# Kernel optimization log

Measured on AMD Instinct MI355X. Metric: run time of the kernel, lower is better.

Reference implementation:

```python
import jax, jax.numpy as jnp
import numpy as np

N_ATOMS = 100000
N_PAIRS = 4000000
N_TYPES = 200
# atom_description columns
AT_NAME, RESNUM, CHAIN = 0, 1, 2
# atom_Properties columns
P_CHARGED, P_CHARGE, P_VIRTUAL, P_DIPOLE, P_RADIUS = 0, 1, 2, 3, 4
# atom-name hash codes (stand-ins for hashings.atom_hash entries)
PHE_RC, TYR_RC, ARG_CZ, ARG_ARG = 10, 11, 12, 13
TEMPERATURE = 298.0
CONSTANT = float(np.exp(-0.004314 * (TEMPERATURE - 273.0)))
DIELEC = 8.8
ION_CORR = 0.02 + 0.05 / 1.4  # Ionic_corrected
PAD = 999.0  # PADDING_INDEX
MAX_DISTANCE = 15.0
KON_APPROACH = 6.0
SOLV_DIELEC = 88.0
RAD10 = float(np.radians(10.0))
RAD30 = float(np.radians(30.0))
RAD150 = float(np.radians(150.0))
RAD180 = float(np.radians(180.0))


def setup_inputs() -> dict:
    key = jax.random.key(0)
    k = jax.random.split(key, 10)
    coords = jax.random.normal(k[0], (N_ATOMS, 3), jnp.float32) * 10.0
    partners = jax.random.normal(k[1], (N_ATOMS, 2, 3), jnp.float32) * 10.0
    at_name = jax.random.randint(k[2], (N_ATOMS,), 0, N_TYPES)
    resnum = jax.random.randint(k[3], (N_ATOMS,), 0, 500)
    chain = jax.random.randint(k[4], (N_ATOMS,), 0, 4)
    atom_description = jnp.stack([at_name, resnum, chain], axis=-1)
    atomPairs = jax.random.randint(k[5], (N_PAIRS, 2), 0, N_ATOMS)
    charged = jax.random.bernoulli(k[6], 0.4, (N_TYPES,)).astype(jnp.float32)
    charge = jax.random.choice(k[7], jnp.array([-1.0, -0.5, 0.5, 1.0], jnp.float32), (N_TYPES,)) * charged
    virtual = jax.random.bernoulli(k[8], 0.1, (N_TYPES,)).astype(jnp.float32)
    kd, kr = jax.random.split(k[9])
    dipole = jax.random.bernoulli(kd, 0.3, (N_TYPES,)).astype(jnp.float32)
    radius = jax.random.uniform(kr, (N_TYPES,), jnp.float32, 1.2, 2.2)
    atom_Properties = jnp.stack([charged, charge, virtual, dipole, radius], axis=-1)
    return {"coords": coords, "partners": partners, "atom_Properties": atom_Properties,
            "atom_description": atom_description, "atomPairs": atomPairs}


def _electro_energy(coords, partners, atom_Properties, atom_description, atomPairs):
    i = atomPairs[:, 0]
    j = atomPairs[:, 1]
    at1 = atom_description[i, AT_NAME]
    at2 = atom_description[j, AT_NAME]

    rc1 = (at1 == PHE_RC) | (at1 == TYR_RC)
    rc2 = (at2 == PHE_RC) | (at2 == TYR_RC)
    argInvolved = ((at1 == ARG_CZ) & ((at2 == ARG_CZ) | rc2)) | ((at2 == ARG_CZ) & ((at1 == ARG_CZ) | rc1))

    charged1 = atom_Properties[at1, P_CHARGED] == 1
    charged2 = atom_Properties[at2, P_CHARGED] == 1
    # NcpMask/CcpMask are all-False (calculate_helical_dipoles == False branch)
    is_charged = (charged1 & charged2) | argInvolved

    diff = coords[i] - coords[j]
    dist = jnp.sqrt(jnp.sum(diff * diff, axis=-1) + 1e-12)  # [P]

    same_res = (atom_description[i, RESNUM] != atom_description[j, RESNUM]) | \
               (atom_description[i, CHAIN] != atom_description[j, CHAIN])
    valid = is_charged & (dist <= MAX_DISTANCE) & same_res  # is_charged_mask & first_mask

    c1 = atom_Properties[at1, P_CHARGE]
    c2 = atom_Properties[at2, P_CHARGE]
    v1 = atom_Properties[at1, P_VIRTUAL] == 1
    v2 = atom_Properties[at2, P_VIRTUAL] == 1
    # hDipoleInvolved is all-False, so the helix-dipole term contributes 0
    charged_charged = valid & (c1 != 0) & (c2 != 0) & (c1 != PAD) & (c2 != PAD) & (~v1) & (~v2)

    # ---- ARG stacking term (plane angle between the two guanidinium/ring planes)
    pA0 = partners[i, 0]; pA1 = partners[i, 1]; cA = coords[i]
    pB0 = partners[j, 0]; pB1 = partners[j, 1]; cB = coords[j]
    n1 = jnp.cross(pA0 - cA, pA1 - cA)
    n2 = jnp.cross(pB0 - cB, pB1 - cB)
    nn1 = jnp.sqrt(jnp.sum(n1 * n1, axis=-1) + 1e-12)
    nn2 = jnp.sqrt(jnp.sum(n2 * n2, axis=-1) + 1e-12)
    m = (nn1 > 1e-6) & (nn2 > 1e-6)
    cosang = jnp.clip(jnp.sum(n1 * n2, axis=-1) / (nn1 * nn2), -0.999999, 0.999999)
    ang = jnp.arccos(cosang)
    ang_bad = ((ang > RAD30) & (ang < RAD150)) | (dist < 3.9) | (dist > 4.3) | (~m)
    arg_mask = valid & argInvolved & (~ang_bad)

    dsafe = jnp.maximum(dist, 1e-6)
    argEpss = 332.0 / (dsafe * DIELEC * CONSTANT)
    temp_d = 3.0 + jnp.abs(dist - 4.1)
    angCorr = dist > RAD150  # faithful to source: distance compared against radians(150)
    corr_ang = jnp.where(angCorr,
                         jnp.maximum((RAD180 - ang) / RAD10, 1.0),
                         jnp.maximum(dist / RAD10, 1.0))
    arg_arg = (at1 == ARG_ARG) & (at2 == ARG_ARG)
    c1e = jnp.ones_like(dist)
    c2e = jnp.where(arg_arg, -1.0, -0.5)
    vk = jnp.sqrt(200.0 * jnp.abs(c1e * c2e) * ION_CORR / TEMPERATURE)
    argE = (1.0 / corr_ang) * c1e * c2e * argEpss * jnp.exp(-temp_d * vk) / (temp_d * temp_d)

    # ---- kon (association-rate electrostatics) term, inter-chain non-dipole charges
    dip1 = atom_Properties[at1, P_DIPOLE] == 0
    dip2 = atom_Properties[at2, P_DIPOLE] == 0
    inter_chain = atom_description[i, CHAIN] != atom_description[j, CHAIN]
    kon_mask = charged_charged & dip1 & dip2 & inter_chain
    sum_radii = atom_Properties[at1, P_RADIUS] + atom_Properties[at2, P_RADIUS] - 0.09
    dd = jnp.maximum(dist, sum_radii)
    temp_kon = jnp.maximum(dd + dd * dd / 30.0, KON_APPROACH)
    IONSTRENGTH = 0.05
    k_on = jnp.sqrt(200.0 * jnp.abs(c1) * jnp.abs(c2) * IONSTRENGTH / TEMPERATURE)
    firstNumber = 332.0 * c1 * c2 / (SOLV_DIELEC * temp_kon * CONSTANT)
    secondNumber = jnp.exp(-k_on * (temp_kon - KON_APPROACH))
    thirdSecond = 1.0 + k_on * KON_APPROACH
    konE = 0.5 * firstNumber * secondNumber / thirdSecond

    zero = jnp.zeros_like(dist)
    virtual_energy = jnp.where(arg_mask, argE, zero) + jnp.where(kon_mask, konE, zero)
    return virtual_energy  # [P], zero at pairs the torch code compacted away


def reference(coords, partners, atom_Properties, atom_description, atomPairs):
    return _electro_energy(coords, partners, atom_Properties, atom_description, atomPairs)
```

## Files before the change

kernel.cpp:

```cpp
#include <hip/hip_runtime.h>
#include <math.h>

namespace {
constexpr int   NTYPES   = 200;
constexpr float RAD10_   = 0.17453292519943295f;
constexpr float RAD30_   = 0.52359877559829882f;
constexpr float RAD150_  = 2.6179938779914944f;
constexpr float RAD180_  = 3.14159265358979323f;
constexpr float CONST_T  = 0.89776110649108887f;

constexpr float ARG_K   = 42.0237329f;
constexpr float KON_K   = 2.10118664f;
constexpr float KON_SQK = 0.18318583f;
constexpr float VK_AA   = 0.19337050f;
constexpr float VK_MIX  = 0.13673360f;

constexpr unsigned RC_B   = 1u << 19;
constexpr unsigned CZ_B   = 1u << 20;
constexpr unsigned AA_B   = 1u << 21;
constexpr unsigned CHG_B  = 1u << 22;
constexpr unsigned VIRT_B = 1u << 23;
constexpr unsigned DIP0_B = 1u << 24;
constexpr unsigned MAG_B  = 1u << 25;
constexpr unsigned SGN_B  = 1u << 26;
constexpr unsigned RESCH_M = 0x7FF00u;
constexpr unsigned CHAIN_M = 0x300u;

constexpr int MAX_FILT_WORDS = 3200;
}

__global__ __launch_bounds__(256) void prep_all(
    const float* __restrict__ coords,
    const float* __restrict__ props,
    const int*   __restrict__ desc,
    float4*      __restrict__ rec,
    unsigned*    __restrict__ filt,
    int nwords, int natoms)
{
    const int idx = blockIdx.x * blockDim.x + threadIdx.x;
    bool interesting = false;
    if (idx < natoms) {
        const int at  = desc[3 * idx];
        const int res = desc[3 * idx + 1];
        const int ch  = desc[3 * idx + 2];
        unsigned bits = (unsigned)at | ((unsigned)ch << 8) | ((unsigned)res << 10);
        if ((at == 10) | (at == 11))       bits |= RC_B;
        if (at == 12)                      bits |= CZ_B;
        if (at == 13)                      bits |= AA_B;
        const float c = props[5 * at + 1];
        if (props[5 * at + 0] == 1.0f)     bits |= CHG_B;
        if (props[5 * at + 2] == 1.0f)     bits |= VIRT_B;
        if (props[5 * at + 3] == 0.0f)     bits |= DIP0_B;
        if (fabsf(c) == 1.0f)              bits |= MAG_B;
        if (c < 0.0f)                      bits |= SGN_B;
        rec[idx] = make_float4(coords[3 * idx], coords[3 * idx + 1],
                               coords[3 * idx + 2], __uint_as_float(bits));
        interesting = ((bits & CHG_B) != 0) | ((bits & (CZ_B | RC_B)) != 0);
    }
    const unsigned long long m = __ballot(interesting);
    const unsigned lane = threadIdx.x & 63u;
    if ((lane & 31u) == 0u) {
        const int w = idx >> 5;
        if (w < nwords) filt[w] = (unsigned)(m >> lane);
    }
}

__device__ __forceinline__ float pe(
    const float4 A, const float4 B, int i, int j,
    const float* __restrict__ partners)
{
    const unsigned ba = __float_as_uint(A.w);
    const unsigned bb = __float_as_uint(B.w);

    const float dx = A.x - B.x, dy = A.y - B.y, dz = A.z - B.z;
    const float dist = sqrtf(dx * dx + dy * dy + dz * dz + 1e-12f);
    const bool diff_res = ((ba ^ bb) & RESCH_M) != 0;
    if (!((dist <= 15.0f) & diff_res)) return 0.0f;

    float energy = 0.0f;

    const bool czA = (ba & CZ_B) != 0, czB = (bb & CZ_B) != 0;
    const bool rcA = (ba & RC_B) != 0, rcB = (bb & RC_B) != 0;
    const bool argInv = (czA & (czB | rcB)) | (czB & (czA | rcA));
    if (argInv && (dist >= 3.9f) && (dist <= 4.3f)) {
        const float a0x = partners[6 * i],     a0y = partners[6 * i + 1], a0z = partners[6 * i + 2];
        const float a1x = partners[6 * i + 3], a1y = partners[6 * i + 4], a1z = partners[6 * i + 5];
        const float b0x = partners[6 * j],     b0y = partners[6 * j + 1], b0z = partners[6 * j + 2];
        const float b1x = partners[6 * j + 3], b1y = partners[6 * j + 4], b1z = partners[6 * j + 5];
        const float u1x = a0x - A.x, u1y = a0y - A.y, u1z = a0z - A.z;
        const float v1x = a1x - A.x, v1y = a1y - A.y, v1z = a1z - A.z;
        const float n1x = u1y * v1z - u1z * v1y;
        const float n1y = u1z * v1x - u1x * v1z;
        const float n1z = u1x * v1y - u1y * v1x;
        const float u2x = b0x - B.x, u2y = b0y - B.y, u2z = b0z - B.z;
        const float v2x = b1x - B.x, v2y = b1y - B.y, v2z = b1z - B.z;
        const float n2x = u2y * v2z - u2z * v2y;
        const float n2y = u2z * v2x - u2x * v2z;
        const float n2z = u2x * v2y - u2y * v2x;
        const float nn1 = sqrtf(n1x * n1x + n1y * n1y + n1z * n1z + 1e-12f);
        const float nn2 = sqrtf(n2x * n2x + n2y * n2y + n2z * n2z + 1e-12f);
        const bool  m = (nn1 > 1e-6f) & (nn2 > 1e-6f);
        float cosang = (n1x * n2x + n1y * n2y + n1z * n2z) / (nn1 * nn2);
        cosang = fminf(fmaxf(cosang, -0.999999f), 0.999999f);
        const float ang = acosf(cosang);
        const bool ang_mid_bad = (ang > RAD30_) & (ang < RAD150_);
        if (m & !ang_mid_bad) {
            const float temp_d = 3.0f + fabsf(dist - 4.1f);
            const float corr = fmaxf((RAD180_ - ang) * (1.0f / RAD10_), 1.0f);
            const bool  arg_arg = ((ba & bb & AA_B) != 0);
            const float c2e = arg_arg ? -1.0f : -0.5f;
            const float vk  = arg_arg ? VK_AA : VK_MIX;
            energy += c2e * ARG_K * expf(-temp_d * vk) /
                      (corr * dist * temp_d * temp_d);
        }
    }

    const bool kon = ((ba & bb & CHG_B) != 0) &
                     (((ba | bb) & VIRT_B) == 0) &
                     ((ba & bb & DIP0_B) != 0) &
                     (((ba ^ bb) & CHAIN_M) != 0);
    if (kon) {
        const float tk = fmaxf(dist + dist * dist * (1.0f / 30.0f), 6.0f);
        const int ms = (int)((ba >> 25) & 1u) + (int)((bb >> 25) & 1u);
        const float mag  = (ms == 0) ? 0.25f : ((ms == 1) ? 0.5f : 1.0f);
        const float k_on = KON_SQK * ((ms == 0) ? 0.5f : ((ms == 1) ? 0.70710678f : 1.0f));
        const float e = KON_K * mag * expf(-k_on * (tk - 6.0f)) /
                        (tk * (1.0f + 6.0f * k_on));
        energy += (((ba ^ bb) & SGN_B) != 0) ? -e : e;
    }
    return energy;
}

__global__ __launch_bounds__(256, 6) void electro_k9(
    const float4*   __restrict__ rec,
    const unsigned* __restrict__ filtg,
    const float*    __restrict__ partners,
    const int*      __restrict__ pairs_raw,
    float*          __restrict__ out,
    int n, int nwords)
{
    __shared__ unsigned sfilt[MAX_FILT_WORDS];
    for (int t = threadIdx.x; t < nwords; t += 256) sfilt[t] = filtg[t];
    __syncthreads();

    const int p0 = blockIdx.x * 512 + 2 * (int)threadIdx.x;
    int i0 = 0, j0 = 0, i1 = 0, j1 = 0;
    if (p0 + 1 < n) {
        const int4 v = *reinterpret_cast<const int4*>(pairs_raw + 2 * p0);
        i0 = v.x; j0 = v.y; i1 = v.z; j1 = v.w;
    } else if (p0 < n) {
        i0 = pairs_raw[2 * p0]; j0 = pairs_raw[2 * p0 + 1];
    }

    const bool f0 = (((sfilt[i0 >> 5] >> (i0 & 31)) & (sfilt[j0 >> 5] >> (j0 & 31))) & 1u) != 0;
    const bool f1 = (((sfilt[i1 >> 5] >> (i1 & 31)) & (sfilt[j1 >> 5] >> (j1 & 31))) & 1u) != 0;

    const int a0 = f0 ? i0 : 0, b0 = f0 ? j0 : 0;
    const int a1 = f1 ? i1 : 0, b1 = f1 ? j1 : 0;

    const float4 A0 = rec[a0];
    const float4 B0 = rec[b0];
    const float4 A1 = rec[a1];
    const float4 B1 = rec[b1];

    const float e0 = f0 ? pe(A0, B0, i0, j0, partners) : 0.0f;
    const float e1 = f1 ? pe(A1, B1, i1, j1, partners) : 0.0f;

    if (p0 + 1 < n) {
        *reinterpret_cast<float2*>(out + p0) = make_float2(e0, e1);
    } else if (p0 < n) {
        out[p0] = e0;
    }
}

__global__ __launch_bounds__(256) void electro_fallback(
    const float* __restrict__ coords, const float* __restrict__ partners,
    const float* __restrict__ props, const int* __restrict__ desc,
    const int2* __restrict__ pairs, float* __restrict__ out, int n)
{
    __shared__ float sp[NTYPES * 5];
    for (int t = threadIdx.x; t < NTYPES * 5; t += blockDim.x) sp[t] = props[t];
    __syncthreads();
    const int stride = gridDim.x * blockDim.x;
    for (int p = blockIdx.x * blockDim.x + threadIdx.x; p < n; p += stride) {
        const int2 ij = pairs[p];
        const int i = ij.x, j = ij.y;
        const int at1 = desc[3 * i], at2 = desc[3 * j];
        const bool rc1 = (at1 == 10) | (at1 == 11);
        const bool rc2 = (at2 == 10) | (at2 == 11);
        const bool argInv = ((at1 == 12) & ((at2 == 12) | rc2)) |
                            ((at2 == 12) & ((at1 == 12) | rc1));
        const float* p1 = &sp[5 * at1];
        const float* p2 = &sp[5 * at2];
        const bool is_charged = ((p1[0] == 1.0f) & (p2[0] == 1.0f)) | argInv;
        float energy = 0.0f;
        if (is_charged) {
            const int res1 = desc[3 * i + 1], ch1 = desc[3 * i + 2];
            const int res2 = desc[3 * j + 1], ch2 = desc[3 * j + 2];
            const float ax = coords[3 * i], ay = coords[3 * i + 1], az = coords[3 * i + 2];
            const float bx = coords[3 * j], by = coords[3 * j + 1], bz = coords[3 * j + 2];
            const float dx = ax - bx, dy = ay - by, dz = az - bz;
            const float dist = sqrtf(dx * dx + dy * dy + dz * dz + 1e-12f);
            const bool diff_res = (res1 != res2) | (ch1 != ch2);
            if ((dist <= 15.0f) & diff_res) {
                if (argInv && (dist >= 3.9f) && (dist <= 4.3f)) {
                    const float a0x = partners[6*i],   a0y = partners[6*i+1], a0z = partners[6*i+2];
                    const float a1x = partners[6*i+3], a1y = partners[6*i+4], a1z = partners[6*i+5];
                    const float b0x = partners[6*j],   b0y = partners[6*j+1], b0z = partners[6*j+2];
                    const float b1x = partners[6*j+3], b1y = partners[6*j+4], b1z = partners[6*j+5];
                    const float u1x=a0x-ax,u1y=a0y-ay,u1z=a0z-az;
                    const float v1x=a1x-ax,v1y=a1y-ay,v1z=a1z-az;
                    const float n1x=u1y*v1z-u1z*v1y, n1y=u1z*v1x-u1x*v1z, n1z=u1x*v1y-u1y*v1x;
                    const float u2x=b0x-bx,u2y=b0y-by,u2z=b0z-bz;
                    const float v2x=b1x-bx,v2y=b1y-by,v2z=b1z-bz;
                    const float n2x=u2y*v2z-u2z*v2y, n2y=u2z*v2x-u2x*v2z, n2z=u2x*v2y-u2y*v2x;
                    const float nn1 = sqrtf(n1x*n1x+n1y*n1y+n1z*n1z+1e-12f);
                    const float nn2 = sqrtf(n2x*n2x+n2y*n2y+n2z*n2z+1e-12f);
                    const bool m = (nn1 > 1e-6f) & (nn2 > 1e-6f);
                    float cosang = (n1x*n2x+n1y*n2y+n1z*n2z)/(nn1*nn2);
                    cosang = fminf(fmaxf(cosang, -0.999999f), 0.999999f);
                    const float ang = acosf(cosang);
                    const bool ang_mid_bad = (ang > RAD30_) & (ang < RAD150_);
                    if (m & !ang_mid_bad) {
                        const float dsafe = fmaxf(dist, 1e-6f);
                        const float argEpss = 332.0f / (dsafe * 8.8f * CONST_T);
                        const float temp_d = 3.0f + fabsf(dist - 4.1f);
                        const float corr_ang = (dist > RAD150_)
                            ? fmaxf((RAD180_ - ang) / RAD10_, 1.0f)
                            : fmaxf(dist / RAD10_, 1.0f);
                        const bool arg_arg = (at1 == 13) & (at2 == 13);
                        const float c2e = arg_arg ? -1.0f : -0.5f;
                        const float vk = sqrtf(200.0f * fabsf(c2e) * (0.02f + 0.05f/1.4f) / 298.0f);
                        energy += (1.0f/corr_ang)*c2e*argEpss*expf(-temp_d*vk)/(temp_d*temp_d);
                    }
                }
                const float c1 = p1[1], c2 = p2[1];
                const bool cc = (c1 != 0.0f) & (c2 != 0.0f) &
                                (p1[2] != 1.0f) & (p2[2] != 1.0f);
                const bool kon_mask = cc & (p1[3] == 0.0f) & (p2[3] == 0.0f) & (ch1 != ch2);
                if (kon_mask) {
                    const float sum_radii = p1[4] + p2[4] - 0.09f;
                    const float dd = fmaxf(dist, sum_radii);
                    const float tk = fmaxf(dd + dd*dd*(1.0f/30.0f), 6.0f);
                    const float k_on = sqrtf(200.0f*fabsf(c1)*fabsf(c2)*0.05f/298.0f);
                    const float first = 332.0f*c1*c2/(88.0f*tk*CONST_T);
                    const float second = expf(-k_on*(tk-6.0f));
                    const float third = 1.0f + k_on*6.0f;
                    energy += 0.5f*first*second/third;
                }
            }
        }
        out[p] = energy;
    }
}

extern "C" void kernel_launch(void* const* d_in, const int* in_sizes, int n_in,
                              void* d_out, int out_size, void* d_ws, size_t ws_size,
                              hipStream_t stream) {
    const float* coords   = (const float*)d_in[0];
    const float* partners = (const float*)d_in[1];
    const float* props    = (const float*)d_in[2];
    const int*   desc     = (const int*)d_in[3];
    const int*   pairs_i  = (const int*)d_in[4];
    float*       out      = (float*)d_out;

    const int natoms = in_sizes[0] / 3;
    const int n      = in_sizes[4] / 2;
    const int nwords = (natoms + 31) / 32;

    const size_t rec_bytes  = (size_t)natoms * sizeof(float4);
    const size_t filt_off   = (rec_bytes + 255) & ~(size_t)255;
    const size_t need_bytes = filt_off + (size_t)nwords * sizeof(unsigned);

    if (ws_size >= need_bytes && nwords <= MAX_FILT_WORDS) {
        float4*   rec  = (float4*)d_ws;
        unsigned* filt = (unsigned*)((char*)d_ws + filt_off);
        prep_all<<<(natoms + 255) / 256, 256, 0, stream>>>(
            coords, props, desc, rec, filt, nwords, natoms);
        const int grid = (n + 511) / 512;
        electro_k9<<<grid, 256, 0, stream>>>(rec, filt, partners, pairs_i, out, n, nwords);
    } else {
        const int block = 256;
        int grid = (n + block - 1) / block;
        if (grid > 2048) grid = 2048;
        electro_fallback<<<grid, block, 0, stream>>>(coords, partners, props,
                                                     desc, (const int2*)pairs_i, out, n);
    }
}
```

Measured before the change: 33.11 us.

## Use persistent grid-stride blocks with prefetched pair tiles and nontemporal I/O

Replaces the one-tile-per-block launch with a capped persistent grid of 2560 blocks that loop over 512-pair tiles. Each block prefetches the next tile's pair indices while it evaluates the current one. The shared-memory filter bitmap is loaded once per block using vectorized loads, where before every one of roughly 7800 blocks reloaded it. Pair loads and output stores use nontemporal hints to avoid polluting the cache, in exchange for less parallelism per launch and slightly more register pressure.

Measured after the change: 30.48 us. 1.09x faster.

```diff
diff --git a/kernel.cpp b/kernel.cpp
--- a/kernel.cpp
+++ b/kernel.cpp
@@ -28,6 +28,9 @@
 
 constexpr int MAX_FILT_WORDS = 3200;
 }
+
+typedef int   i4v __attribute__((ext_vector_type(4)));
+typedef float f2v __attribute__((ext_vector_type(2)));
 
 __global__ __launch_bounds__(256) void prep_all(
     const float* __restrict__ coords,
@@ -131,45 +134,76 @@
     return energy;
 }
 
-__global__ __launch_bounds__(256, 6) void electro_k9(
+__global__ __launch_bounds__(256, 6) void electro_k11(
     const float4*   __restrict__ rec,
     const unsigned* __restrict__ filtg,
     const float*    __restrict__ partners,
     const int*      __restrict__ pairs_raw,
     float*          __restrict__ out,
-    int n, int nwords)
+    int n, int nwords, int tiles)
 {
     __shared__ unsigned sfilt[MAX_FILT_WORDS];
-    for (int t = threadIdx.x; t < nwords; t += 256) sfilt[t] = filtg[t];
+    {
+        const uint4* fsrc = reinterpret_cast<const uint4*>(filtg);
+        const int nv = nwords >> 2;
+        for (int t = threadIdx.x; t < nv; t += 256) {
+            const uint4 v = fsrc[t];
+            sfilt[4 * t]     = v.x;  sfilt[4 * t + 1] = v.y;
+            sfilt[4 * t + 2] = v.z;  sfilt[4 * t + 3] = v.w;
+        }
+        for (int t = (nv << 2) + threadIdx.x; t < nwords; t += 256)
+            sfilt[t] = filtg[t];
+    }
     __syncthreads();
 
-    const int p0 = blockIdx.x * 512 + 2 * (int)threadIdx.x;
-    int i0 = 0, j0 = 0, i1 = 0, j1 = 0;
-    if (p0 + 1 < n) {
-        const int4 v = *reinterpret_cast<const int4*>(pairs_raw + 2 * p0);
-        i0 = v.x; j0 = v.y; i1 = v.z; j1 = v.w;
-    } else if (p0 < n) {
-        i0 = pairs_raw[2 * p0]; j0 = pairs_raw[2 * p0 + 1];
-    }
-
-    const bool f0 = (((sfilt[i0 >> 5] >> (i0 & 31)) & (sfilt[j0 >> 5] >> (j0 & 31))) & 1u) != 0;
-    const bool f1 = (((sfilt[i1 >> 5] >> (i1 & 31)) & (sfilt[j1 >> 5] >> (j1 & 31))) & 1u) != 0;
-
-    const int a0 = f0 ? i0 : 0, b0 = f0 ? j0 : 0;
-    const int a1 = f1 ? i1 : 0, b1 = f1 ? j1 : 0;
-
-    const float4 A0 = rec[a0];
-    const float4 B0 = rec[b0];
-    const float4 A1 = rec[a1];
-    const float4 B1 = rec[b1];
-
-    const float e0 = f0 ? pe(A0, B0, i0, j0, partners) : 0.0f;
-    const float e1 = f1 ? pe(A1, B1, i1, j1, partners) : 0.0f;
-
-    if (p0 + 1 < n) {
-        *reinterpret_cast<float2*>(out + p0) = make_float2(e0, e1);
-    } else if (p0 < n) {
-        out[p0] = e0;
+    const int tid = (int)threadIdx.x;
+
+    auto load_tile = [&](int tile) -> i4v {
+        const int p = (tile << 9) + 2 * tid;
+        if (p + 1 < n)
+            return __builtin_nontemporal_load(
+                reinterpret_cast<const i4v*>(pairs_raw + 2 * p));
+        i4v r = (i4v)0;
+        if (p < n) { r.x = pairs_raw[2 * p]; r.y = pairs_raw[2 * p + 1]; }
+        return r;
+    };
+
+    int tile = blockIdx.x;
+    if (tile >= tiles) return;
+    i4v cur = load_tile(tile);
+
+    while (true) {
+        const int next = tile + gridDim.x;
+        i4v nxt = (i4v)0;
+        if (next < tiles) nxt = load_tile(next);
+
+        const int p0 = (tile << 9) + 2 * tid;
+        const int i0 = cur.x, j0 = cur.y, i1 = cur.z, j1 = cur.w;
+
+        const bool f0 = (((sfilt[i0 >> 5] >> (i0 & 31)) & (sfilt[j0 >> 5] >> (j0 & 31))) & 1u) != 0;
+        const bool f1 = (((sfilt[i1 >> 5] >> (i1 & 31)) & (sfilt[j1 >> 5] >> (j1 & 31))) & 1u) != 0;
+
+        const int a0 = f0 ? i0 : 0, b0 = f0 ? j0 : 0;
+        const int a1 = f1 ? i1 : 0, b1 = f1 ? j1 : 0;
+
+        const float4 A0 = rec[a0];
+        const float4 B0 = rec[b0];
+        const float4 A1 = rec[a1];
+        const float4 B1 = rec[b1];
+
+        const float e0 = f0 ? pe(A0, B0, i0, j0, partners) : 0.0f;
+        const float e1 = f1 ? pe(A1, B1, i1, j1, partners) : 0.0f;
+
+        if (p0 + 1 < n) {
+            f2v r; r.x = e0; r.y = e1;
+            __builtin_nontemporal_store(r, reinterpret_cast<f2v*>(out + p0));
+        } else if (p0 < n) {
+            out[p0] = e0;
+        }
+
+        if (next >= tiles) break;
+        tile = next;
+        cur  = nxt;
     }
 }
 
@@ -277,8 +311,10 @@
         unsigned* filt = (unsigned*)((char*)d_ws + filt_off);
         prep_all<<<(natoms + 255) / 256, 256, 0, stream>>>(
             coords, props, desc, rec, filt, nwords, natoms);
-        const int grid = (n + 511) / 512;
-        electro_k9<<<grid, 256, 0, stream>>>(rec, filt, partners, pairs_i, out, n, nwords);
+        const int tiles = (n + 511) / 512;
+        int grid = tiles < 2560 ? tiles : 2560;
+        electro_k11<<<grid, 256, 0, stream>>>(rec, filt, partners, pairs_i,
+                                              out, n, nwords, tiles);
     } else {
         const int block = 256;
         int grid = (n + block - 1) / block;
```
